# Performance work log

Measured on AMD Instinct MI355X. Metric: run time of the kernel, lower is better.

The kernel has to match this reference:

```python
import jax, jax.numpy as jnp
import numpy as np

MARGIN = 0.2
ENCODER_STRIDE = 320


def setup_inputs() -> dict:
    key = jax.random.key(0)
    k1, k2, k3, k4 = jax.random.split(key, 4)
    B, D, T, NC = 8, 512, 2048, 4096
    student_features = jax.random.normal(k1, (B, D, T), dtype=jnp.float32)
    codebook = jax.random.normal(k2, (NC, D), dtype=jnp.float32)
    teacher_codes = jax.random.randint(k3, (B, T), 0, NC, dtype=jnp.int64)
    lengths = jax.random.randint(k4, (B,), 0, T * ENCODER_STRIDE, dtype=jnp.int64)
    return {
        "student_features": student_features,
        "teacher_codes": teacher_codes,
        "codebook": codebook,
        "lengths": lengths,
    }


def reference(student_features, teacher_codes, codebook, lengths):
    B, D, T = student_features.shape
    # frame-level valid mask: (B, T)
    frame_lengths = lengths // ENCODER_STRIDE
    mask = (jnp.arange(T)[None, :] < frame_lengths[:, None]).astype(student_features.dtype)

    # (B*T, D) flattened student vectors
    z = jnp.transpose(student_features, (0, 2, 1)).reshape(-1, D)

    # Euclidean cdist via ||z||^2 + ||c||^2 - 2 z c^T (matmul form, like torch.cdist)
    sq = (
        jnp.sum(z * z, axis=-1, keepdims=True)
        + jnp.sum(codebook * codebook, axis=-1)[None, :]
        - 2.0 * jnp.einsum("nd,cd->nc", z, codebook)
    )
    dists = jnp.sqrt(jnp.maximum(sq, 1e-12))  # (B*T, num_codes)

    teacher_flat = teacher_codes.reshape(-1)
    rows = jnp.arange(teacher_flat.shape[0])
    pos_dist = dists[rows, teacher_flat]
    # exclude the target code, then min over codebook
    dists_for_neg = dists.at[rows, teacher_flat].set(jnp.inf)
    neg_dist = jnp.min(dists_for_neg, axis=1)

    triplet = jax.nn.relu(pos_dist.reshape(B, T) - neg_dist.reshape(B, T) + MARGIN)
    loss = jnp.sum(triplet * mask) / (jnp.sum(mask) + 1e-8)
    return loss
```

## Files before the change

kernel.cpp:

```cpp
#include <hip/hip_runtime.h>
#include <hip/hip_bf16.h>

typedef float f32x4 __attribute__((ext_vector_type(4)));
typedef int v8i __attribute__((ext_vector_type(8)));

#define NB 8
#define ND 512
#define NT 2048
#define NCODES 4096
#define NM (NB * NT)
#define MARGIN_F 0.2f
#define ENC_STRIDE 320


static __device__ inline void async_copy16(const void* g, void* l) {
    __builtin_amdgcn_global_load_lds(
        (const __attribute__((address_space(1))) unsigned int*)g,
        (__attribute__((address_space(3))) unsigned int*)l, 16, 0, 0);
}

static __device__ inline bool rank_decode(const int* __restrict__ lengths, int rank,
                                          int shift, int& b, int& tib) {
    int acc = 0;
    bool ok = false;
#pragma unroll
    for (int bb = 0; bb < NB; bb++) {
        int fl = lengths[bb] / ENC_STRIDE;
        int c = (fl + ((1 << shift) - 1)) >> shift;
        if (!ok && rank < acc + c) { b = bb; tib = rank - acc; ok = true; }
        acc += c;
    }
    return ok;
}

__global__ void prep_fused(const float* __restrict__ sf, const float* __restrict__ cb,
                           const int* __restrict__ lengths,
                           unsigned char* __restrict__ Zq, float* __restrict__ npart,
                           unsigned char* __restrict__ Cq, float* __restrict__ cnorm,
                           float* __restrict__ accum, unsigned int* __restrict__ ticket) {
    __shared__ float tile[128][65];
    __shared__ float redc[4][16];
    const int tid = threadIdx.x;
    const int wave = tid >> 6, lane = tid & 63, l15 = lane & 15, kq = lane >> 4;

    if (blockIdx.x < 1024) {
        const int bx = blockIdx.x;
        int b, tt;
        if (!rank_decode(lengths, bx >> 2, 6, b, tt)) return;
        const int t0 = tt * 64;
        const int d0 = (bx & 3) * 128;
        const float* src = sf + (size_t)b * ND * NT;
#pragma unroll
        for (int it = 0; it < 8; it++) {
            int idx = it * 256 + tid;
            int d = idx >> 4, t4 = (idx & 15) * 4;
            float4 v = *(const float4*)(src + (size_t)(d0 + d) * NT + t0 + t4);
            tile[d][t4] = v.x; tile[d][t4 + 1] = v.y; tile[d][t4 + 2] = v.z; tile[d][t4 + 3] = v.w;
        }
        __syncthreads();
        const int m0 = b * NT + t0;
        {
            const int trow = wave * 16 + l15;
            unsigned char q[32];
#pragma unroll
            for (int j = 0; j < 32; j += 2) {
                float a = tile[kq * 32 + j][trow];
                float c = tile[kq * 32 + j + 1][trow];
                int p = __builtin_amdgcn_cvt_pk_fp8_f32(a, c, 0, false);
                q[j] = (unsigned char)(p & 0xFF);
                q[j + 1] = (unsigned char)((p >> 8) & 0xFF);
            }
            const int M_ = m0 >> 7, rg = ((m0 >> 4) & 7) + wave, K_ = d0 >> 7;
            char* base = (char*)Zq + ((size_t)((M_ * 4 + K_) * 8 + rg)) * 2048;
            *(uint4*)(base + lane * 16) = *(uint4*)&q[0];
            *(uint4*)(base + 1024 + lane * 16) = *(uint4*)&q[16];
        }
        if (tid < 64) {
            float s = 0.0f;
#pragma unroll 16
            for (int d = 0; d < 128; d++) {
                float v = tile[d][tid];
                s += v * v;
            }
            npart[(size_t)(d0 >> 7) * NM + m0 + tid] = s;
        }
    } else {
        if (blockIdx.x == 1279 && tid == 0) { *accum = 0.0f; *ticket = 0u; }
        const int r0 = (blockIdx.x - 1024) * 16;
        const int row = r0 + l15;
        const int K_ = wave;
        const float* src = cb + (size_t)row * ND + K_ * 128 + kq * 32;
        unsigned char q[32];
        float s = 0.0f;
#pragma unroll
        for (int j4 = 0; j4 < 8; j4++) {
            float4 v = *(const float4*)(src + j4 * 4);
            s += v.x * v.x + v.y * v.y + v.z * v.z + v.w * v.w;
            int p0 = __builtin_amdgcn_cvt_pk_fp8_f32(v.x, v.y, 0, false);
            int p1 = __builtin_amdgcn_cvt_pk_fp8_f32(v.z, v.w, 0, false);
            q[j4 * 4 + 0] = (unsigned char)(p0 & 0xFF);
            q[j4 * 4 + 1] = (unsigned char)((p0 >> 8) & 0xFF);
            q[j4 * 4 + 2] = (unsigned char)(p1 & 0xFF);
            q[j4 * 4 + 3] = (unsigned char)((p1 >> 8) & 0xFF);
        }
        const int N_ = r0 >> 7, rg = (r0 >> 4) & 7;
        char* base = (char*)Cq + ((size_t)((N_ * 4 + K_) * 8 + rg)) * 2048;
        *(uint4*)(base + lane * 16) = *(uint4*)&q[0];
        *(uint4*)(base + 1024 + lane * 16) = *(uint4*)&q[16];
        s += __shfl_xor(s, 16);
        s += __shfl_xor(s, 32);
        if (lane < 16) redc[wave][l15] = s;
        __syncthreads();
        if (tid < 16) cnorm[r0 + tid] = redc[0][tid] + redc[1][tid] + redc[2][tid] + redc[3][tid];
    }
}

__global__ __launch_bounds__(256, 2) void triplet_main(
    const unsigned char* __restrict__ Zq, const unsigned char* __restrict__ Cq,
    const float* __restrict__ cnorm, const int* __restrict__ teacher,
    const int* __restrict__ lengths,
    float* __restrict__ negq, float* __restrict__ posq) {
    __shared__ __align__(16) unsigned char As[2][16384];
    __shared__ __align__(16) unsigned char Bs[2][16384];

    int b, tM;
    if (!rank_decode(lengths, (int)blockIdx.x >> 3, 7, b, tM)) return;
    const int nq = blockIdx.x & 7;
    const int M_ = b * 16 + tM;
    const int m0 = M_ * 128;

    const int tid = threadIdx.x;
    const int wave = tid >> 6, lane = tid & 63;
    const int wr = wave >> 1, wc = wave & 1;
    const int l15 = lane & 15, quad = lane >> 4;

    const float INF = __builtin_inff();
    float minv[4][4], posv[4][4];
    int tch[4][4];
#pragma unroll
    for (int mi = 0; mi < 4; mi++)
#pragma unroll
        for (int r = 0; r < 4; r++) {
            minv[mi][r] = INF;
            posv[mi][r] = INF;
            tch[mi][r] = teacher[m0 + wr * 64 + mi * 16 + quad * 4 + r];
        }

    const int ldsoff = wave * 4096;
    const char* gA0 = (const char*)Zq + (size_t)M_ * 4 * 16384 + ldsoff + lane * 16;
    const char* gB0 = (const char*)Cq + (size_t)nq * 16 * 16384 + ldsoff + lane * 16;

#pragma unroll
    for (int i = 0; i < 4; i++) {
        async_copy16(gA0 + i * 1024, (char*)As[0] + ldsoff + i * 1024);
        async_copy16(gB0 + i * 1024, (char*)Bs[0] + ldsoff + i * 1024);
    }
    __syncthreads();

    f32x4 acc[4][4];
    int cur = 0;
#pragma unroll 2
    for (int u = 0; u < 16; ++u) {
        const int nt = u >> 2, kt = u & 3;
        if (kt == 0) {
#pragma unroll
            for (int mi = 0; mi < 4; mi++)
#pragma unroll
                for (int ni = 0; ni < 4; ni++)
                    acc[mi][ni] = (f32x4){0.f, 0.f, 0.f, 0.f};
        }
        if (u < 15) {
            const int un = u + 1;
            const char* gA = gA0 + (size_t)(un & 3) * 16384;
            const char* gB = gB0 + (size_t)un * 16384;
            char* dA = (char*)As[cur ^ 1] + ldsoff;
            char* dB = (char*)Bs[cur ^ 1] + ldsoff;
#pragma unroll
            for (int i = 0; i < 4; i++) {
                async_copy16(gA + i * 1024, dA + i * 1024);
                async_copy16(gB + i * 1024, dB + i * 1024);
            }
        }

        const unsigned char* sA = As[cur];
        const unsigned char* sB = Bs[cur];
        v8i av[4], bv[4];
#pragma unroll
        for (int mi = 0; mi < 4; mi++) {
            int rg = wr * 4 + mi;
            union { uint4 q[2]; v8i v; } uu;
            uu.q[0] = *(const uint4*)(sA + rg * 2048 + lane * 16);
            uu.q[1] = *(const uint4*)(sA + rg * 2048 + 1024 + lane * 16);
            av[mi] = uu.v;
        }
#pragma unroll
        for (int ni = 0; ni < 4; ni++) {
            int rg = wc * 4 + ni;
            union { uint4 q[2]; v8i v; } uu;
            uu.q[0] = *(const uint4*)(sB + rg * 2048 + lane * 16);
            uu.q[1] = *(const uint4*)(sB + rg * 2048 + 1024 + lane * 16);
            bv[ni] = uu.v;
        }
#pragma unroll
        for (int mi = 0; mi < 4; mi++)
#pragma unroll
            for (int ni = 0; ni < 4; ni++)
                acc[mi][ni] = __builtin_amdgcn_mfma_scale_f32_16x16x128_f8f6f4(
                    av[mi], bv[ni], acc[mi][ni], 0, 0,
                    0, 0x7F7F7F7F, 0, 0x7F7F7F7F);

        if (kt == 3) {
            const int n0 = (nq * 4 + nt) * 128;
            float cn[4]; int col[4];
#pragma unroll
            for (int ni = 0; ni < 4; ni++) {
                col[ni] = n0 + wc * 64 + ni * 16 + l15;
                cn[ni] = cnorm[col[ni]];
            }
#pragma unroll
            for (int mi = 0; mi < 4; mi++)
#pragma unroll
                for (int r = 0; r < 4; r++) {
                    int t = tch[mi][r];
#pragma unroll
                    for (int ni = 0; ni < 4; ni++) {
                        float val = fmaf(-2.0f, acc[mi][ni][r], cn[ni]);
                        bool ist = (col[ni] == t);
                        minv[mi][r] = fminf(minv[mi][r], ist ? INF : val);
                        posv[mi][r] = fminf(posv[mi][r], ist ? val : INF);
                    }
                }
        }
        __syncthreads();
        cur ^= 1;
    }

    const int slot = nq * 2 + wc;
#pragma unroll
    for (int mi = 0; mi < 4; mi++)
#pragma unroll
        for (int r = 0; r < 4; r++) {
            float mn = minv[mi][r], ps = posv[mi][r];
#pragma unroll
            for (int off = 1; off < 16; off <<= 1) {
                mn = fminf(mn, __shfl_xor(mn, off));
                ps = fminf(ps, __shfl_xor(ps, off));
            }
            if (l15 == 0) {
                int m = m0 + wr * 64 + mi * 16 + quad * 4 + r;
                negq[(size_t)slot * NM + m] = mn;
                posq[(size_t)slot * NM + m] = ps;
            }
        }
}

__global__ void reduce_final(const float* __restrict__ negq, const float* __restrict__ posq,
                             const float* __restrict__ npart, const int* __restrict__ lengths,
                             float* __restrict__ accum, unsigned int* __restrict__ ticket,
                             float* __restrict__ out) {
    const float INF = __builtin_inff();
    const int m = blockIdx.x * 256 + threadIdx.x;
    float mn = INF, ps = INF;
#pragma unroll
    for (int s = 0; s < 16; s++) {
        mn = fminf(mn, negq[(size_t)s * NM + m]);
        ps = fminf(ps, posq[(size_t)s * NM + m]);
    }
    float zn = npart[m] + npart[NM + m] + npart[2 * NM + m] + npart[3 * NM + m];
    float negd = sqrtf(fmaxf(zn + mn, 1e-12f));
    float posd = sqrtf(fmaxf(zn + ps, 1e-12f));
    float tri = fmaxf(posd - negd + MARGIN_F, 0.0f);
    int b = m >> 11;
    int tt = m & (NT - 1);
    int flen = lengths[b] / ENC_STRIDE;
    float val = (tt < flen) ? tri : 0.0f;

    __shared__ float red[4];
#pragma unroll
    for (int off = 1; off < 64; off <<= 1) val += __shfl_xor(val, off);
    int lane = threadIdx.x & 63, w = threadIdx.x >> 6;
    if (lane == 0) red[w] = val;
    __syncthreads();
    if (threadIdx.x == 0) {
        atomicAdd(accum, red[0] + red[1] + red[2] + red[3]);
        __threadfence();
        unsigned int old = atomicAdd(ticket, 1u);
        if (old == 63u) {
            float total = atomicAdd(accum, 0.0f);
            float cnt = 0.0f;
            for (int bb = 0; bb < NB; bb++) cnt += (float)(lengths[bb] / ENC_STRIDE);
            out[0] = total / (cnt + 1e-8f);
        }
    }
}

extern "C" void kernel_launch(void* const* d_in, const int* in_sizes, int n_in,
                              void* d_out, int out_size, void* d_ws, size_t ws_size,
                              hipStream_t stream) {
    const float* sf = (const float*)d_in[0];
    const int* teacher = (const int*)d_in[1];
    const float* cb = (const float*)d_in[2];
    const int* lengths = (const int*)d_in[3];

    char* ws = (char*)d_ws;
    unsigned char* Zq = (unsigned char*)(ws);
    unsigned char* Cq = (unsigned char*)(ws + 8388608);
    float* cnorm = (float*)(ws + 10485760);
    float* npart = (float*)(ws + 10502144);
    float* negq = (float*)(ws + 10764288);
    float* posq = (float*)(ws + 11812864);
    float* accum = (float*)(ws + 12861440);
    unsigned int* ticket = (unsigned int*)(ws + 12861444);

    prep_fused<<<1280, 256, 0, stream>>>(sf, cb, lengths, Zq, npart, Cq, cnorm, accum, ticket);
    triplet_main<<<1024, 256, 0, stream>>>(Zq, Cq, cnorm, teacher, lengths, negq, posq);
    reduce_final<<<64, 256, 0, stream>>>(negq, posq, npart, lengths, accum, ticket,
                                         (float*)d_out);
}
```

Measured before the change: 133.4 us.

## Load MFMA operands directly from global memory, dropping LDS double buffering

```diff
diff --git a/kernel.cpp b/kernel.cpp
--- a/kernel.cpp
+++ b/kernel.cpp
@@ -12,12 +12,6 @@
 #define MARGIN_F 0.2f
 #define ENC_STRIDE 320
 
-
-static __device__ inline void async_copy16(const void* g, void* l) {
-    __builtin_amdgcn_global_load_lds(
-        (const __attribute__((address_space(1))) unsigned int*)g,
-        (__attribute__((address_space(3))) unsigned int*)l, 16, 0, 0);
-}
 
 static __device__ inline bool rank_decode(const int* __restrict__ lengths, int rank,
                                           int shift, int& b, int& tib) {
@@ -120,9 +114,6 @@
     const float* __restrict__ cnorm, const int* __restrict__ teacher,
     const int* __restrict__ lengths,
     float* __restrict__ negq, float* __restrict__ posq) {
-    __shared__ __align__(16) unsigned char As[2][16384];
-    __shared__ __align__(16) unsigned char Bs[2][16384];
-
     int b, tM;
     if (!rank_decode(lengths, (int)blockIdx.x >> 3, 7, b, tM)) return;
     const int nq = blockIdx.x & 7;
@@ -146,93 +137,66 @@
             tch[mi][r] = teacher[m0 + wr * 64 + mi * 16 + quad * 4 + r];
         }
 
-    const int ldsoff = wave * 4096;
-    const char* gA0 = (const char*)Zq + (size_t)M_ * 4 * 16384 + ldsoff + lane * 16;
-    const char* gB0 = (const char*)Cq + (size_t)nq * 16 * 16384 + ldsoff + lane * 16;
-
-#pragma unroll
-    for (int i = 0; i < 4; i++) {
-        async_copy16(gA0 + i * 1024, (char*)As[0] + ldsoff + i * 1024);
-        async_copy16(gB0 + i * 1024, (char*)Bs[0] + ldsoff + i * 1024);
-    }
-    __syncthreads();
-
-    f32x4 acc[4][4];
-    int cur = 0;
-#pragma unroll 2
-    for (int u = 0; u < 16; ++u) {
-        const int nt = u >> 2, kt = u & 3;
-        if (kt == 0) {
+    const char* gA = (const char*)Zq + (size_t)(M_ * 4) * 16384 + (wr * 4) * 2048 + lane * 16;
+    const char* gB = (const char*)Cq + (size_t)(nq * 16) * 16384 + (wc * 4) * 2048 + lane * 16;
+
+#pragma unroll 1
+    for (int nt = 0; nt < 4; ++nt) {
+        f32x4 acc[4][4];
+#pragma unroll
+        for (int mi = 0; mi < 4; mi++)
+#pragma unroll
+            for (int ni = 0; ni < 4; ni++)
+                acc[mi][ni] = (f32x4){0.f, 0.f, 0.f, 0.f};
+
+#pragma unroll
+        for (int kt = 0; kt < 4; ++kt) {
+            const char* pA = gA + (size_t)kt * 16384;
+            const char* pB = gB + (size_t)(nt * 4 + kt) * 16384;
+            v8i av[4], bv[4];
+#pragma unroll
+            for (int mi = 0; mi < 4; mi++) {
+                union { uint4 q[2]; v8i v; } uu;
+                uu.q[0] = *(const uint4*)(pA + mi * 2048);
+                uu.q[1] = *(const uint4*)(pA + mi * 2048 + 1024);
+                av[mi] = uu.v;
+            }
+#pragma unroll
+            for (int ni = 0; ni < 4; ni++) {
+                union { uint4 q[2]; v8i v; } uu;
+                uu.q[0] = *(const uint4*)(pB + ni * 2048);
+                uu.q[1] = *(const uint4*)(pB + ni * 2048 + 1024);
+                bv[ni] = uu.v;
+            }
 #pragma unroll
             for (int mi = 0; mi < 4; mi++)
 #pragma unroll
                 for (int ni = 0; ni < 4; ni++)
-                    acc[mi][ni] = (f32x4){0.f, 0.f, 0.f, 0.f};
-        }
-        if (u < 15) {
-            const int un = u + 1;
-            const char* gA = gA0 + (size_t)(un & 3) * 16384;
-            const char* gB = gB0 + (size_t)un * 16384;
-            char* dA = (char*)As[cur ^ 1] + ldsoff;
-            char* dB = (char*)Bs[cur ^ 1] + ldsoff;
-#pragma unroll
-            for (int i = 0; i < 4; i++) {
-                async_copy16(gA + i * 1024, dA + i * 1024);
-                async_copy16(gB + i * 1024, dB + i * 1024);
-            }
-        }
-
-        const unsigned char* sA = As[cur];
-        const unsigned char* sB = Bs[cur];
-        v8i av[4], bv[4];
-#pragma unroll
-        for (int mi = 0; mi < 4; mi++) {
-            int rg = wr * 4 + mi;
-            union { uint4 q[2]; v8i v; } uu;
-            uu.q[0] = *(const uint4*)(sA + rg * 2048 + lane * 16);
-            uu.q[1] = *(const uint4*)(sA + rg * 2048 + 1024 + lane * 16);
-            av[mi] = uu.v;
-        }
+                    acc[mi][ni] = __builtin_amdgcn_mfma_scale_f32_16x16x128_f8f6f4(
+                        av[mi], bv[ni], acc[mi][ni], 0, 0,
+                        0, 0x7F7F7F7F, 0, 0x7F7F7F7F);
+        }
+
+        const int n0 = (nq * 4 + nt) * 128;
+        float cn[4]; int col[4];
 #pragma unroll
         for (int ni = 0; ni < 4; ni++) {
-            int rg = wc * 4 + ni;
-            union { uint4 q[2]; v8i v; } uu;
-            uu.q[0] = *(const uint4*)(sB + rg * 2048 + lane * 16);
-            uu.q[1] = *(const uint4*)(sB + rg * 2048 + 1024 + lane * 16);
-            bv[ni] = uu.v;
+            col[ni] = n0 + wc * 64 + ni * 16 + l15;
+            cn[ni] = cnorm[col[ni]];
         }
 #pragma unroll
         for (int mi = 0; mi < 4; mi++)
 #pragma unroll
-            for (int ni = 0; ni < 4; ni++)
-                acc[mi][ni] = __builtin_amdgcn_mfma_scale_f32_16x16x128_f8f6f4(
-                    av[mi], bv[ni], acc[mi][ni], 0, 0,
-                    0, 0x7F7F7F7F, 0, 0x7F7F7F7F);
-
-        if (kt == 3) {
-            const int n0 = (nq * 4 + nt) * 128;
-            float cn[4]; int col[4];
-#pragma unroll
-            for (int ni = 0; ni < 4; ni++) {
-                col[ni] = n0 + wc * 64 + ni * 16 + l15;
-                cn[ni] = cnorm[col[ni]];
-            }
-#pragma unroll
-            for (int mi = 0; mi < 4; mi++)
-#pragma unroll
-                for (int r = 0; r < 4; r++) {
-                    int t = tch[mi][r];
-#pragma unroll
-                    for (int ni = 0; ni < 4; ni++) {
-                        float val = fmaf(-2.0f, acc[mi][ni][r], cn[ni]);
-                        bool ist = (col[ni] == t);
-                        minv[mi][r] = fminf(minv[mi][r], ist ? INF : val);
-                        posv[mi][r] = fminf(posv[mi][r], ist ? val : INF);
-                    }
+            for (int r = 0; r < 4; r++) {
+                int t = tch[mi][r];
+#pragma unroll
+                for (int ni = 0; ni < 4; ni++) {
+                    float val = fmaf(-2.0f, acc[mi][ni][r], cn[ni]);
+                    bool ist = (col[ni] == t);
+                    minv[mi][r] = fminf(minv[mi][r], ist ? INF : val);
+                    posv[mi][r] = fminf(posv[mi][r], ist ? val : INF);
                 }
-        }
-        __syncthreads();
-        cur ^= 1;
+            }
     }
 
     const int slot = nq * 2 + wc;
```

Result: slower. 243.7 us (+82.8%).
